# Performance work log

Hardware: AMD Instinct MI355X
Metric: run time of the kernel (lower is better)

The kernel has to match this reference:

```python
import jax, jax.numpy as jnp
import numpy as np

D_MODEL = 1024
NUM_HEAD = 16
BATCH = 2
SEQ = 2048
NEG_INF = -1e9  # matches masked_fill value in the original


def setup_inputs() -> dict:
    key = jax.random.key(0)
    k1, k2, k3, k4, k5 = jax.random.split(key, 5)
    scale = 1.0 / np.sqrt(D_MODEL)
    return {
        "x": jax.random.normal(k1, (BATCH, SEQ, D_MODEL), dtype=jnp.float32),
        "q_weight": jax.random.normal(k2, (D_MODEL, D_MODEL), dtype=jnp.float32) * scale,
        "k_weight": jax.random.normal(k3, (D_MODEL, D_MODEL), dtype=jnp.float32) * scale,
        "v_weight": jax.random.normal(k4, (D_MODEL, D_MODEL), dtype=jnp.float32) * scale,
        "o_weight": jax.random.normal(k5, (D_MODEL, D_MODEL), dtype=jnp.float32) * scale,
    }


def reference(x, q_weight, k_weight, v_weight, o_weight):
    b, s, d = x.shape
    h = NUM_HEAD
    dh = d // h
    # projections: weight layout is (d_out, d_in)
    q = jnp.einsum('bsd,ed->bse', x, q_weight).reshape(b, s, h, dh).transpose(0, 2, 1, 3)
    k = jnp.einsum('bsd,ed->bse', x, k_weight).reshape(b, s, h, dh).transpose(0, 2, 1, 3)
    v = jnp.einsum('bsd,ed->bse', x, v_weight).reshape(b, s, h, dh).transpose(0, 2, 1, 3)
    scores = jnp.einsum('bhqd,bhkd->bhqk', q, k) / jnp.sqrt(jnp.asarray(dh, x.dtype))
    causal = jnp.triu(jnp.ones((s, s), dtype=bool), k=1)  # True above diagonal -> masked
    scores = jnp.where(causal, jnp.asarray(NEG_INF, x.dtype), scores)
    attn = jax.nn.softmax(scores, axis=-1)
    out = jnp.einsum('bhqk,bhkd->bhqd', attn, v)          # [b,h,s,dh]
    out = out.transpose(0, 2, 1, 3).reshape(b, s, d)       # merge heads
    return jnp.einsum('bse,de->bsd', out, o_weight)
```

## Files before the change

kernel.cpp:

```cpp
#include <hip/hip_runtime.h>

typedef short bhalf8 __attribute__((ext_vector_type(8)));
typedef float floatx4 __attribute__((ext_vector_type(4)));

#define D_MODEL 1024
#define SEQ     2048
#define BATCH   2
#define NHEAD   16
#define DH      64

#define GLDS(g, l) __builtin_amdgcn_global_load_lds( \
    (const __attribute__((address_space(1))) void*)(g), \
    (__attribute__((address_space(3))) void*)(l), 16, 0, 0)

static __device__ __forceinline__ short f2bf(float f) {
    unsigned u = __builtin_bit_cast(unsigned, f);
    u = (u + 0x7fffu + ((u >> 16) & 1u)) >> 16;
    return (short)u;
}
static __device__ __forceinline__ unsigned pack2(float a, float b) {
    return (unsigned)(unsigned short)f2bf(a) | ((unsigned)(unsigned short)f2bf(b) << 16);
}
static __device__ __forceinline__ unsigned cvt_pk_bf16(float lo, float hi) {
    unsigned r;
    asm("v_cvt_pk_bf16_f32 %0, %1, %2" : "=v"(r) : "v"(lo), "v"(hi));
    return r;
}

__global__ __launch_bounds__(256) void cast_x(const float* __restrict__ s,
                                              short* __restrict__ d) {
    int i = (blockIdx.x * 256 + threadIdx.x) * 8;
    float4 a = *(const float4*)(s + i);
    float4 b = *(const float4*)(s + i + 4);
    uint4 u = {pack2(a.x, a.y), pack2(a.z, a.w), pack2(b.x, b.y), pack2(b.z, b.w)};
    *(uint4*)(d + i) = u;
}

__global__ __launch_bounds__(256) void cast_w(const float* __restrict__ wq,
                                              const float* __restrict__ wk,
                                              const float* __restrict__ wv,
                                              const float* __restrict__ wo,
                                              short* __restrict__ dst) {
    const float* s = (blockIdx.y == 0) ? wq : (blockIdx.y == 1) ? wk
                   : (blockIdx.y == 2) ? wv : wo;
    size_t off = (size_t)blockIdx.y * (D_MODEL * D_MODEL);
    int i = (blockIdx.x * 256 + threadIdx.x) * 8;
    float4 a = *(const float4*)(s + i);
    float4 b = *(const float4*)(s + i + 4);
    uint4 u = {pack2(a.x, a.y), pack2(a.z, a.w), pack2(b.x, b.y), pack2(b.z, b.w)};
    *(uint4*)(dst + off + i) = u;
}

__global__ __launch_bounds__(256) void gemm_qkv(const short* __restrict__ A,
                                                const short* __restrict__ W,
                                                short* __restrict__ Qo,
                                                short* __restrict__ Ko,
                                                short* __restrict__ Vt) {
    __shared__ __align__(16) char pool[34816];
    short (*As)[64] = (short(*)[64])pool;
    short (*Bs)[64] = (short(*)[64])(pool + 16384);
    const int t    = threadIdx.x;
    const int wave = t >> 6, lane = t & 63, quad = lane >> 4, l16 = lane & 15;
    const int bm = blockIdx.x * 128, by = blockIdx.y, bn = by * 128;
    const int qm = (wave >> 1) * 64, qn = (wave & 1) * 64;

    const int lrow = lane >> 3, lcol = (lane & 7) * 8;
    const short* Ag = A + (size_t)(bm + wave * 32 + lrow) * 1024 + lcol;
    const short* Wg = W + (size_t)(bn + wave * 32 + lrow) * 1024 + lcol;
    short* Al = &As[wave * 32][0];
    short* Bl = &Bs[wave * 32][0];

    floatx4 acc[4][4];
#pragma unroll
    for (int i = 0; i < 4; ++i)
#pragma unroll
        for (int j = 0; j < 4; ++j) {
            floatx4 z = {0.f, 0.f, 0.f, 0.f};
            acc[i][j] = z;
        }

    for (int k0 = 0; k0 < 1024; k0 += 64) {
        __syncthreads();
#pragma unroll
        for (int j = 0; j < 4; ++j) {
            GLDS(Ag + k0 + (size_t)j * 8 * 1024, Al + j * 8 * 64);
            GLDS(Wg + k0 + (size_t)j * 8 * 1024, Bl + j * 8 * 64);
        }
        __syncthreads();
#pragma unroll
        for (int kk = 0; kk < 64; kk += 32) {
            bhalf8 af[4], bfr[4];
#pragma unroll
            for (int im = 0; im < 4; ++im)
                af[im] = *(const bhalf8*)&As[qm + im * 16 + l16][kk + quad * 8];
#pragma unroll
            for (int jn = 0; jn < 4; ++jn)
                bfr[jn] = *(const bhalf8*)&Bs[qn + jn * 16 + l16][kk + quad * 8];
#pragma unroll
            for (int im = 0; im < 4; ++im)
#pragma unroll
                for (int jn = 0; jn < 4; ++jn)
                    acc[im][jn] = __builtin_amdgcn_mfma_f32_16x16x32_bf16(
                        af[im], bfr[jn], acc[im][jn], 0, 0, 0);
        }
    }

    __syncthreads();
    short (*Ct)[136] = (short(*)[136])pool;
    const bool isV = (by >= 16);
#pragma unroll
    for (int im = 0; im < 4; ++im)
#pragma unroll
        for (int jn = 0; jn < 4; ++jn)
#pragma unroll
            for (int g = 0; g < 4; ++g) {
                const int ml = qm + im * 16 + quad * 4 + g;
                const int nl = qn + jn * 16 + l16;
                if (isV) Ct[nl][ml] = f2bf(acc[im][jn][g]);
                else     Ct[ml][nl] = f2bf(acc[im][jn][g]);
            }
    __syncthreads();

    short* outp;
    size_t rowbase, colbase, stride;
    if (by < 8)       { outp = Qo; rowbase = bm;                colbase = bn;        stride = 1024; }
    else if (by < 16) { outp = Ko; rowbase = bm;                colbase = bn - 1024; stride = 1024; }
    else              { outp = Vt; rowbase = (size_t)bn - 2048; colbase = bm;        stride = 4096; }
#pragma unroll
    for (int pass = 0; pass < 8; ++pass) {
        const int r = (t >> 4) + pass * 16;
        const int c = (t & 15) * 8;
        uint4 u = *(const uint4*)&Ct[r][c];
        *(uint4*)(outp + (rowbase + r) * stride + colbase + c) = u;
    }
}

__global__ __launch_bounds__(256) void gemm_o(const short* __restrict__ A,
                                              const short* __restrict__ W,
                                              float* __restrict__ C) {
    __shared__ __align__(16) char pool[34816];
    short (*As)[64] = (short(*)[64])pool;
    short (*Bs)[64] = (short(*)[64])(pool + 16384);
    const int t    = threadIdx.x;
    const int wave = t >> 6, lane = t & 63, quad = lane >> 4, l16 = lane & 15;
    const int bm = blockIdx.x * 128, bn = blockIdx.y * 64;
    const int qm = (wave >> 1) * 64, qn = (wave & 1) * 32;

    const int lrow = lane >> 3, lcol = (lane & 7) * 8;
    const short* Ag = A + (size_t)(bm + wave * 32 + lrow) * 1024 + lcol;
    const short* Wg = W + (size_t)(bn + wave * 16 + lrow) * 1024 + lcol;
    short* Al = &As[wave * 32][0];
    short* Bl = &Bs[wave * 16][0];

    floatx4 acc[4][2];
#pragma unroll
    for (int i = 0; i < 4; ++i)
#pragma unroll
        for (int j = 0; j < 2; ++j) {
            floatx4 z = {0.f, 0.f, 0.f, 0.f};
            acc[i][j] = z;
        }

    for (int k0 = 0; k0 < 1024; k0 += 64) {
        __syncthreads();
#pragma unroll
        for (int j = 0; j < 4; ++j)
            GLDS(Ag + k0 + (size_t)j * 8 * 1024, Al + j * 8 * 64);
#pragma unroll
        for (int j = 0; j < 2; ++j)
            GLDS(Wg + k0 + (size_t)j * 8 * 1024, Bl + j * 8 * 64);
        __syncthreads();
#pragma unroll
        for (int kk = 0; kk < 64; kk += 32) {
            bhalf8 af[4], bfr[2];
#pragma unroll
            for (int im = 0; im < 4; ++im)
                af[im] = *(const bhalf8*)&As[qm + im * 16 + l16][kk + quad * 8];
#pragma unroll
            for (int jn = 0; jn < 2; ++jn)
                bfr[jn] = *(const bhalf8*)&Bs[qn + jn * 16 + l16][kk + quad * 8];
#pragma unroll
            for (int im = 0; im < 4; ++im)
#pragma unroll
                for (int jn = 0; jn < 2; ++jn)
                    acc[im][jn] = __builtin_amdgcn_mfma_f32_16x16x32_bf16(
                        af[im], bfr[jn], acc[im][jn], 0, 0, 0);
        }
    }

    __syncthreads();
    float (*Ctf)[68] = (float(*)[68])pool;
#pragma unroll
    for (int im = 0; im < 4; ++im)
#pragma unroll
        for (int jn = 0; jn < 2; ++jn)
#pragma unroll
            for (int g = 0; g < 4; ++g)
                Ctf[qm + im * 16 + quad * 4 + g][qn + jn * 16 + l16] = acc[im][jn][g];
    __syncthreads();
#pragma unroll
    for (int pass = 0; pass < 8; ++pass) {
        const int r = (t >> 4) + pass * 16;
        const int c = (t & 15) * 4;
        float4 u = *(const float4*)&Ctf[r][c];
        *(float4*)(C + (size_t)(bm + r) * 1024 + bn + c) = u;
    }
}

#define MFMA_BF16 __builtin_amdgcn_mfma_f32_16x16x32_bf16

#define STAGE_LOAD(kregv, vregv, kk) do {                                     \
    kregv = *(const uint4*)(Kbase + (size_t)((kk) + sr) * 1024 + sc);         \
    vregv = *(const uint4*)(Vbase + (size_t)sr * 4096 + (kk) + sc);           \
    } while (0)

#define STAGE_WRITE(bufv, kregv, vregv) do {                                  \
    *(uint4*)&Ks[bufv][sr][sc] = kregv;                                       \
    *(uint4*)&Vs[bufv][sr][sc] = vregv;                                       \
    } while (0)

#define CHUNK13(bufv, k0v, qwv) do {                                          \
    bhalf8 kf_[4][2];                                                         \
    _Pragma("unroll")                                                         \
    for (int jn_ = 0; jn_ < 4; ++jn_) {                                       \
        kf_[jn_][0] = *(const bhalf8*)&Ks[bufv][jn_ * 16 + l16][quad * 8];    \
        kf_[jn_][1] = *(const bhalf8*)&Ks[bufv][jn_ * 16 + l16][32 + quad * 8]; \
    }                                                                         \
    floatx4 s_[4];                                                            \
    _Pragma("unroll")                                                         \
    for (int jn_ = 0; jn_ < 4; ++jn_) {                                       \
        floatx4 z_ = {0.f, 0.f, 0.f, 0.f};                                    \
        z_ = MFMA_BF16(qf0, kf_[jn_][0], z_, 0, 0, 0);                        \
        z_ = MFMA_BF16(qf1, kf_[jn_][1], z_, 0, 0, 0);                        \
        s_[jn_] = z_;                                                         \
    }                                                                         \
    bhalf8 vf_[4][2];              \
    _Pragma("unroll")                                                         \
    for (int nd_ = 0; nd_ < 4; ++nd_) {                                       \
        vf_[nd_][0] = *(const bhalf8*)&Vs[bufv][nd_ * 16 + l16][quad * 8];    \
        vf_[nd_][1] = *(const bhalf8*)&Vs[bufv][nd_ * 16 + l16][32 + quad * 8]; \
    }                                                                         \
    const bool partial_ = ((k0v) + 64 > (qwv));                               \
    _Pragma("unroll")                                                         \
    for (int g_ = 0; g_ < 4; ++g_) {                                          \
        const int rr_ = quad * 4 + g_;                                        \
        const int qrow_ = (qwv) + rr_;                                        \
        float e0_ = exp2f(s_[0][g_] * KS - CB);                               \
        float e1_ = exp2f(s_[1][g_] * KS - CB);                               \
        float e2_ = exp2f(s_[2][g_] * KS - CB);                               \
        float e3_ = exp2f(s_[3][g_] * KS - CB);                               \
        if (partial_) {                                                       \
            if ((k0v) + l16 > qrow_)      e0_ = 0.f;                          \
            if ((k0v) + 16 + l16 > qrow_) e1_ = 0.f;                          \
            if ((k0v) + 32 + l16 > qrow_) e2_ = 0.f;                          \
            if ((k0v) + 48 + l16 > qrow_) e3_ = 0.f;                          \
        }                                                                     \
        lsum[g_] += (e0_ + e1_) + (e2_ + e3_);                                \
        unsigned r01_ = cvt_pk_bf16(e0_, e1_);                                \
        unsigned r23_ = cvt_pk_bf16(e2_, e3_);                                \
        Ps[wave][rr_][l16]      = (short)r01_;                                \
        Ps[wave][rr_][16 + l16] = (short)(r01_ >> 16);                        \
        Ps[wave][rr_][32 + l16] = (short)r23_;                                \
        Ps[wave][rr_][48 + l16] = (short)(r23_ >> 16);                        \
    }                                                                         \
          \
    bhalf8 ap0_ = *(const bhalf8*)&Ps[wave][l16][quad * 8];                   \
    bhalf8 ap1_ = *(const bhalf8*)&Ps[wave][l16][32 + quad * 8];              \
    _Pragma("unroll")                                                         \
    for (int nd_ = 0; nd_ < 4; ++nd_) {                                       \
        o[nd_] = MFMA_BF16(ap0_, vf_[nd_][0], o[nd_], 0, 0, 0);               \
        o[nd_] = MFMA_BF16(ap1_, vf_[nd_][1], o[nd_], 0, 0, 0);               \
    }                                                                         \
} while (0)

#define SWEEP(qtv, ncv) do {                                                  \
    const int qw_ = (qtv) * 128 + wave * 16;                                  \
    const short* qr_ = Qbase + (size_t)(qw_ + l16) * 1024;                    \
    bhalf8 qf0 = *(const bhalf8*)(qr_ + quad * 8);                            \
    bhalf8 qf1 = *(const bhalf8*)(qr_ + 32 + quad * 8);                       \
    _Pragma("unroll")                                                         \
    for (int g_ = 0; g_ < 4; ++g_) lsum[g_] = 0.f;                            \
    _Pragma("unroll")                                                         \
    for (int nd_ = 0; nd_ < 4; ++nd_) {                                       \
        floatx4 z_ = {0.f, 0.f, 0.f, 0.f};                                    \
        o[nd_] = z_;                                                          \
    }                                                                         \
    uint4 kreg_, vreg_;                                                       \
    STAGE_LOAD(kreg_, vreg_, 0);                                              \
    STAGE_WRITE(0, kreg_, vreg_);                                             \
    if ((ncv) > 1) STAGE_LOAD(kreg_, vreg_, 64);                              \
    __syncthreads();                                                          \
    _Pragma("unroll 1")                                                       \
    for (int i_ = 0; i_ < (ncv); ++i_) {                                      \
        const int buf_ = i_ & 1;                                              \
        if (i_ + 1 < (ncv)) STAGE_WRITE(buf_ ^ 1, kreg_, vreg_);              \
        if (i_ + 2 < (ncv)) STAGE_LOAD(kreg_, vreg_, (i_ + 2) * 64);          \
        CHUNK13(buf_, i_ * 64, qw_);                                          \
        __syncthreads();                                                      \
    }                                                                         \
    _Pragma("unroll")                                                         \
    for (int g_ = 0; g_ < 4; ++g_) {                                          \
        float r_ = lsum[g_];                                                  \
        r_ += __shfl_xor(r_, 1, 64);                                          \
        r_ += __shfl_xor(r_, 2, 64);                                          \
        r_ += __shfl_xor(r_, 4, 64);                                          \
        r_ += __shfl_xor(r_, 8, 64);                                          \
        const float iv_ = 1.0f / r_;                                          \
        const int qrow_ = qw_ + quad * 4 + g_;                                \
        _Pragma("unroll")                                                     \
        for (int nd_ = 0; nd_ < 4; ++nd_)                                     \
            Y[(size_t)(b * SEQ + qrow_) * 1024 + h * 64 + nd_ * 16 + l16] =   \
                f2bf(o[nd_][g_] * iv_);                                       \
    }                                                                         \
} while (0)

__global__ __launch_bounds__(512) void attn_v14(const short* __restrict__ Qo,
                                                const short* __restrict__ Ko,
                                                const short* __restrict__ Vt,
                                                short* __restrict__ Y) {
    __shared__ __align__(16) short Ks[2][64][72];
    __shared__ __align__(16) short Vs[2][64][72];
    __shared__ __align__(16) short Ps[8][16][72];

    const int t    = threadIdx.x;
    const int wave = t >> 6, lane = t & 63, quad = lane >> 4, l16 = lane & 15;
    const int bid  = (int)blockIdx.x;
    const int bh   = bid & 31;
    const int p    = (bid & 255) >> 5;
    const int qt   = (bid < 256) ? (15 - p) : p;
    const int b = bh >> 4, h = bh & 15;

    const short* Qbase = Qo + (size_t)b * SEQ * 1024 + h * 64;
    const short* Kbase = Ko + (size_t)b * SEQ * 1024 + h * 64;
    const short* Vbase = Vt + (size_t)h * 64 * 4096 + (size_t)b * SEQ;

    const int sr = t >> 3;
    const int sc = (t & 7) * 8;

    const float KS = 0.125f * 1.44269504f;
    const float CB = 12.0f * 1.44269504f;

    float lsum[4];
    floatx4 o[4];

    SWEEP(qt, (qt + 1) * 2);
}

extern "C" void kernel_launch(void* const* d_in, const int* in_sizes, int n_in,
                              void* d_out, int out_size, void* d_ws, size_t ws_size,
                              hipStream_t stream) {
    const float* x  = (const float*)d_in[0];
    const float* wq = (const float*)d_in[1];
    const float* wk = (const float*)d_in[2];
    const float* wv = (const float*)d_in[3];
    const float* wo = (const float*)d_in[4];

    short* xb   = (short*)d_ws;
    short* Qo   = xb + (size_t)4096 * 1024;
    short* Ko   = Qo + (size_t)4096 * 1024;
    short* Vt   = Ko + (size_t)4096 * 1024;
    short* wall = Vt + (size_t)1024 * 4096;
    short* wob  = wall + (size_t)3 * 1024 * 1024;

    cast_x<<<dim3(2048), 256, 0, stream>>>(x, xb);
    cast_w<<<dim3(512, 4), 256, 0, stream>>>(wq, wk, wv, wo, wall);
    gemm_qkv<<<dim3(32, 24), 256, 0, stream>>>(xb, wall, Qo, Ko, Vt);
    attn_v14<<<dim3(512), 512, 0, stream>>>(Qo, Ko, Vt, xb);
    gemm_o<<<dim3(32, 16), 256, 0, stream>>>(xb, wob, (float*)d_out);
}
```

Before: 197.3 us.

## Rewrite QKV GEMM with 256x256 tiles and triple-buffered LDS pipeline; merge cast kernels

Replaces the 128x128 QKV projection GEMM with a 512-thread kernel using 256x256 output tiles, K-step 32, and a three-stage global_load_lds pipeline with raised MFMA priority. Also merges the x and weight cast kernels into a single launch. Larger tiles raise operand reuse and cut LDS-load traffic per MFMA, but the grid shrinks to 192 blocks, fewer than the CU count, and the unpadded 32-short LDS rows may cause bank conflicts.

```diff
diff --git a/kernel.cpp b/kernel.cpp
--- a/kernel.cpp
+++ b/kernel.cpp
@@ -27,111 +27,160 @@
     return r;
 }
 
-__global__ __launch_bounds__(256) void cast_x(const float* __restrict__ s,
-                                              short* __restrict__ d) {
-    int i = (blockIdx.x * 256 + threadIdx.x) * 8;
+__global__ __launch_bounds__(256) void cast_all(const float* __restrict__ x,
+                                                const float* __restrict__ wq,
+                                                const float* __restrict__ wk,
+                                                const float* __restrict__ wv,
+                                                const float* __restrict__ wo,
+                                                short* __restrict__ xb,
+                                                short* __restrict__ wall) {
+    const int bid = blockIdx.x;
+    const float* s;
+    short* d;
+    int i;
+    if (bid < 2048) {
+        s = x; d = xb;
+        i = (bid * 256 + threadIdx.x) * 8;
+    } else {
+        const int wb = bid - 2048;
+        const int which = wb >> 9;
+        s = (which == 0) ? wq : (which == 1) ? wk : (which == 2) ? wv : wo;
+        d = wall + (size_t)which * (D_MODEL * D_MODEL);
+        i = ((wb & 511) * 256 + threadIdx.x) * 8;
+    }
     float4 a = *(const float4*)(s + i);
     float4 b = *(const float4*)(s + i + 4);
     uint4 u = {pack2(a.x, a.y), pack2(a.z, a.w), pack2(b.x, b.y), pack2(b.z, b.w)};
     *(uint4*)(d + i) = u;
 }
 
-__global__ __launch_bounds__(256) void cast_w(const float* __restrict__ wq,
-                                              const float* __restrict__ wk,
-                                              const float* __restrict__ wv,
-                                              const float* __restrict__ wo,
-                                              short* __restrict__ dst) {
-    const float* s = (blockIdx.y == 0) ? wq : (blockIdx.y == 1) ? wk
-                   : (blockIdx.y == 2) ? wv : wo;
-    size_t off = (size_t)blockIdx.y * (D_MODEL * D_MODEL);
-    int i = (blockIdx.x * 256 + threadIdx.x) * 8;
-    float4 a = *(const float4*)(s + i);
-    float4 b = *(const float4*)(s + i + 4);
-    uint4 u = {pack2(a.x, a.y), pack2(a.z, a.w), pack2(b.x, b.y), pack2(b.z, b.w)};
-    *(uint4*)(dst + off + i) = u;
-}
-
-__global__ __launch_bounds__(256) void gemm_qkv(const short* __restrict__ A,
-                                                const short* __restrict__ W,
-                                                short* __restrict__ Qo,
-                                                short* __restrict__ Ko,
-                                                short* __restrict__ Vt) {
-    __shared__ __align__(16) char pool[34816];
-    short (*As)[64] = (short(*)[64])pool;
-    short (*Bs)[64] = (short(*)[64])(pool + 16384);
+#define MFMA_BF16 __builtin_amdgcn_mfma_f32_16x16x32_bf16
+
+#define QISSUE(kt, s) do {                                                    \
+    char* ab_ = pool + (s) * 16384 + (w * 32) * 64;                           \
+    char* bb_ = pool + 49152 + (s) * 16384 + (w * 32) * 64;                   \
+    GLDS(Ag + (size_t)(kt) * 32, ab_);                                        \
+    GLDS(Ag + (size_t)(kt) * 32 + 16 * 1024, ab_ + 1024);                     \
+    GLDS(Wg + (size_t)(kt) * 32, bb_);                                        \
+    GLDS(Wg + (size_t)(kt) * 32 + 16 * 1024, bb_ + 1024);                     \
+} while (0)
+
+#define QCOMP(s) do {                                                         \
+    const short(*As_)[32] = (const short(*)[32])(pool + (s) * 16384);         \
+    const short(*Bs_)[32] = (const short(*)[32])(pool + 49152 + (s) * 16384); \
+    bhalf8 af_[8], bf_[4];                                                    \
+    _Pragma("unroll")                                                         \
+    for (int m_ = 0; m_ < 8; ++m_)                                            \
+        af_[m_] = *(const bhalf8*)&As_[wr * 128 + m_ * 16 + l16][quad * 8];   \
+    _Pragma("unroll")                                                         \
+    for (int n_ = 0; n_ < 4; ++n_)                                            \
+        bf_[n_] = *(const bhalf8*)&Bs_[wc * 64 + n_ * 16 + l16][quad * 8];    \
+    __builtin_amdgcn_s_setprio(1);                                            \
+    _Pragma("unroll")                                                         \
+    for (int m_ = 0; m_ < 8; ++m_)                                            \
+        _Pragma("unroll")                                                     \
+        for (int n_ = 0; n_ < 4; ++n_)                                        \
+            acc[m_][n_] = MFMA_BF16(af_[m_], bf_[n_], acc[m_][n_], 0, 0, 0);  \
+    __builtin_amdgcn_s_setprio(0);                                            \
+} while (0)
+
+__global__ __launch_bounds__(512) void gemm_qkv2(const short* __restrict__ A,
+                                                 const short* __restrict__ W,
+                                                 short* __restrict__ Qo,
+                                                 short* __restrict__ Ko,
+                                                 short* __restrict__ Vt) {
+    __shared__ __align__(16) char pool[98304];
     const int t    = threadIdx.x;
-    const int wave = t >> 6, lane = t & 63, quad = lane >> 4, l16 = lane & 15;
-    const int bm = blockIdx.x * 128, by = blockIdx.y, bn = by * 128;
-    const int qm = (wave >> 1) * 64, qn = (wave & 1) * 64;
-
-    const int lrow = lane >> 3, lcol = (lane & 7) * 8;
-    const short* Ag = A + (size_t)(bm + wave * 32 + lrow) * 1024 + lcol;
-    const short* Wg = W + (size_t)(bn + wave * 32 + lrow) * 1024 + lcol;
-    short* Al = &As[wave * 32][0];
-    short* Bl = &Bs[wave * 32][0];
-
-    floatx4 acc[4][4];
-#pragma unroll
-    for (int i = 0; i < 4; ++i)
-#pragma unroll
-        for (int j = 0; j < 4; ++j) {
+    const int w    = t >> 6, lane = t & 63, quad = lane >> 4, l16 = lane & 15;
+    const int wr   = w >> 2, wc = w & 3;
+    const int bm   = blockIdx.x * 256;
+    const int by   = (int)blockIdx.y;
+    const int bn   = by * 256;
+
+    const short* Ag = A + (size_t)(bm + w * 32 + (lane >> 2)) * 1024 + (lane & 3) * 8;
+    const short* Wg = W + (size_t)(bn + w * 32 + (lane >> 2)) * 1024 + (lane & 3) * 8;
+
+    floatx4 acc[8][4];
+#pragma unroll
+    for (int m = 0; m < 8; ++m)
+#pragma unroll
+        for (int n = 0; n < 4; ++n) {
             floatx4 z = {0.f, 0.f, 0.f, 0.f};
-            acc[i][j] = z;
+            acc[m][n] = z;
         }
 
-    for (int k0 = 0; k0 < 1024; k0 += 64) {
-        __syncthreads();
-#pragma unroll
-        for (int j = 0; j < 4; ++j) {
-            GLDS(Ag + k0 + (size_t)j * 8 * 1024, Al + j * 8 * 64);
-            GLDS(Wg + k0 + (size_t)j * 8 * 1024, Bl + j * 8 * 64);
+    QISSUE(0, 0);
+    QISSUE(1, 1);
+    int sc_ = 0, sn_ = 2;
+#pragma unroll 1
+    for (int kt = 0; kt < 30; ++kt) {
+        asm volatile("s_waitcnt vmcnt(4)" ::: "memory");
+        __builtin_amdgcn_s_barrier();
+        QISSUE(kt + 2, sn_);
+        QCOMP(sc_);
+        sc_ = (sc_ == 2) ? 0 : sc_ + 1;
+        sn_ = (sn_ == 2) ? 0 : sn_ + 1;
+    }
+    asm volatile("s_waitcnt vmcnt(4)" ::: "memory");
+    __builtin_amdgcn_s_barrier();
+    QCOMP(sc_);
+    sc_ = (sc_ == 2) ? 0 : sc_ + 1;
+    asm volatile("s_waitcnt vmcnt(0)" ::: "memory");
+    __builtin_amdgcn_s_barrier();
+    QCOMP(sc_);
+
+    __syncthreads();
+    short (*Ct)[268] = (short(*)[268])pool;
+    if (by < 8) {
+        short* outp = (by < 4) ? Qo : Ko;
+        const int colbase = (by < 4) ? bn : bn - 1024;
+        for (int hh = 0; hh < 2; ++hh) {
+            if (wr == hh) {
+#pragma unroll
+                for (int m = 0; m < 8; ++m)
+#pragma unroll
+                    for (int n = 0; n < 4; ++n)
+#pragma unroll
+                        for (int g = 0; g < 4; ++g)
+                            Ct[m * 16 + quad * 4 + g][wc * 64 + n * 16 + l16] =
+                                f2bf(acc[m][n][g]);
+            }
+            __syncthreads();
+            {
+                const int r = t >> 2, c0 = (t & 3) * 64;
+#pragma unroll
+                for (int p = 0; p < 8; ++p)
+                    *(uint4*)(outp + (size_t)(bm + hh * 128 + r) * 1024 +
+                              colbase + c0 + p * 8) =
+                        *(const uint4*)&Ct[r][c0 + p * 8];
+            }
+            __syncthreads();
         }
-        __syncthreads();
-#pragma unroll
-        for (int kk = 0; kk < 64; kk += 32) {
-            bhalf8 af[4], bfr[4];
-#pragma unroll
-            for (int im = 0; im < 4; ++im)
-                af[im] = *(const bhalf8*)&As[qm + im * 16 + l16][kk + quad * 8];
-#pragma unroll
-            for (int jn = 0; jn < 4; ++jn)
-                bfr[jn] = *(const bhalf8*)&Bs[qn + jn * 16 + l16][kk + quad * 8];
-#pragma unroll
-            for (int im = 0; im < 4; ++im)
-#pragma unroll
-                for (int jn = 0; jn < 4; ++jn)
-                    acc[im][jn] = __builtin_amdgcn_mfma_f32_16x16x32_bf16(
-                        af[im], bfr[jn], acc[im][jn], 0, 0, 0);
+    } else {
+        const int nbase = bn - 2048;
+        for (int hh = 0; hh < 2; ++hh) {
+            if ((wc >> 1) == hh) {
+#pragma unroll
+                for (int m = 0; m < 8; ++m)
+#pragma unroll
+                    for (int n = 0; n < 4; ++n)
+#pragma unroll
+                        for (int g = 0; g < 4; ++g)
+                            Ct[wc * 64 + n * 16 + l16 - hh * 128]
+                              [wr * 128 + m * 16 + quad * 4 + g] =
+                                f2bf(acc[m][n][g]);
+            }
+            __syncthreads();
+            {
+                const int r = t >> 2, c0 = (t & 3) * 64;
+#pragma unroll
+                for (int p = 0; p < 8; ++p)
+                    *(uint4*)(Vt + (size_t)(nbase + hh * 128 + r) * 4096 +
+                              bm + c0 + p * 8) =
+                        *(const uint4*)&Ct[r][c0 + p * 8];
+            }
+            __syncthreads();
         }
-    }
-
-    __syncthreads();
-    short (*Ct)[136] = (short(*)[136])pool;
-    const bool isV = (by >= 16);
-#pragma unroll
-    for (int im = 0; im < 4; ++im)
-#pragma unroll
-        for (int jn = 0; jn < 4; ++jn)
-#pragma unroll
-            for (int g = 0; g < 4; ++g) {
-                const int ml = qm + im * 16 + quad * 4 + g;
-                const int nl = qn + jn * 16 + l16;
-                if (isV) Ct[nl][ml] = f2bf(acc[im][jn][g]);
-                else     Ct[ml][nl] = f2bf(acc[im][jn][g]);
-            }
-    __syncthreads();
-
-    short* outp;
-    size_t rowbase, colbase, stride;
-    if (by < 8)       { outp = Qo; rowbase = bm;                colbase = bn;        stride = 1024; }
-    else if (by < 16) { outp = Ko; rowbase = bm;                colbase = bn - 1024; stride = 1024; }
-    else              { outp = Vt; rowbase = (size_t)bn - 2048; colbase = bm;        stride = 4096; }
-#pragma unroll
-    for (int pass = 0; pass < 8; ++pass) {
-        const int r = (t >> 4) + pass * 16;
-        const int c = (t & 15) * 8;
-        uint4 u = *(const uint4*)&Ct[r][c];
-        *(uint4*)(outp + (rowbase + r) * stride + colbase + c) = u;
     }
 }
 
@@ -207,7 +256,6 @@
     }
 }
 
-#define MFMA_BF16 __builtin_amdgcn_mfma_f32_16x16x32_bf16
 
 #define STAGE_LOAD(kregv, vregv, kk) do {                                     \
     kregv = *(const uint4*)(Kbase + (size_t)((kk) + sr) * 1024 + sc);         \
@@ -362,9 +410,8 @@
     short* wall = Vt + (size_t)1024 * 4096;
     short* wob  = wall + (size_t)3 * 1024 * 1024;
 
-    cast_x<<<dim3(2048), 256, 0, stream>>>(x, xb);
-    cast_w<<<dim3(512, 4), 256, 0, stream>>>(wq, wk, wv, wo, wall);
-    gemm_qkv<<<dim3(32, 24), 256, 0, stream>>>(xb, wall, Qo, Ko, Vt);
+    cast_all<<<dim3(4096), 256, 0, stream>>>(x, wq, wk, wv, wo, xb, wall);
+    gemm_qkv2<<<dim3(16, 12), 512, 0, stream>>>(xb, wall, Qo, Ko, Vt);
     attn_v14<<<dim3(512), 512, 0, stream>>>(Qo, Ko, Vt, xb);
     gemm_o<<<dim3(32, 16), 256, 0, stream>>>(xb, wob, (float*)d_out);
 }
```

Result: faster. 190.1 us (-3.6%).
